# Kernel optimization log

Hardware: AMD Instinct MI355X
Metric: run time of the kernel (lower is better)

The kernel has to match this reference:

```python
import jax, jax.numpy as jnp
import numpy as np

N, M = 50000, 24
F_NODE_IN, F_EDGE_IN = 92, 41
F, E = 64, 64  # node_fea_len, edge_fea_len


def _kaiming(key, fan_in, fan_out):
    # kaiming_uniform_(mode='fan_in', nonlinearity='relu'): bound = sqrt(6/fan_in)
    bound = np.sqrt(6.0 / fan_in)
    return jax.random.uniform(key, (fan_in, fan_out), jnp.float32, -bound, bound)


def setup_inputs() -> dict:
    key = jax.random.key(0)
    ks = jax.random.split(key, 10)
    node_fea = jax.random.normal(ks[0], (N, F_NODE_IN), jnp.float32)
    edge_fea = jax.random.normal(ks[1], (N, M, F_EDGE_IN), jnp.float32)
    # indices in [-1, N-1); -1 marks padded neighbors (masked), matching torch semantics
    edge_fea_idx = jax.random.randint(ks[2], (N, M), 0, N + 1, jnp.int64 if jax.config.jax_enable_x64 else jnp.int32) - 1
    inp = {
        'node_fea': node_fea,
        'edge_fea': edge_fea,
        'edge_fea_idx': edge_fea_idx,
        'Wn': _kaiming(ks[3], F_NODE_IN, F), 'bn': jnp.zeros((F,), jnp.float32),
        'We': _kaiming(ks[4], F_EDGE_IN, E), 'be': jnp.zeros((E,), jnp.float32),
    }
    for i, k in zip((1, 2, 3), ks[5:8]):
        inp[f'W{i}'] = _kaiming(k, 2 * F + E, 2 * F)
        inp[f'b{i}'] = jnp.zeros((2 * F,), jnp.float32)
        inp[f'a{i}'] = jnp.float32(0.7)
    return inp


def conv_layer(node, edge, idx, W, b, alpha):
    n, m = idx.shape
    nbr = node[idx]  # (N, M, F) gather; negative idx wraps like torch, masked below
    self_fea = jnp.broadcast_to(node[:, None, :], (n, m, node.shape[-1]))
    total = jnp.concatenate([self_fea, nbr, edge], axis=2)  # (N, M, 2F+E)
    gated = total @ W + b  # (N, M, 2F)
    nbr_filter, nbr_core = jnp.split(gated, 2, axis=2)
    mask = (idx >= 0)[:, :, None].astype(node.dtype)
    prod = jax.nn.sigmoid(nbr_filter) * jax.nn.softplus(nbr_core) * mask
    nbr_sumed = jnp.sum(prod, axis=1)  # (N, F)
    return jax.nn.softplus(alpha * node + nbr_sumed)


def reference(node_fea, edge_fea, edge_fea_idx, Wn, bn, We, be,
              W1, b1, a1, W2, b2, a2, W3, b3, a3):
    node = node_fea @ Wn + bn            # (N, 64)
    edge = edge_fea @ We + be            # (N, M, 64)
    node = conv_layer(node, edge, edge_fea_idx, W1, b1, a1)
    node = conv_layer(node, edge, edge_fea_idx, W2, b2, a2)
    node = conv_layer(node, edge, edge_fea_idx, W3, b3, a3)
    return node
```

## Files before the change

### kernel.cpp

```cpp
#include <hip/hip_runtime.h>
#include <cstdint>
#include <cstddef>

#define NN   50000
#define MM   24
#define FNIN 92
#define FEIN 41
#define NBLK 3125
#define EROW 48
#define ETILE (MM * 16 * EROW)
#define LOG2E 1.4426950408889634f
#define LN2   0.6931471805599453f

typedef __attribute__((ext_vector_type(8))) short bf16x8;
typedef __attribute__((ext_vector_type(4))) float f32x4;
typedef __attribute__((ext_vector_type(8))) unsigned short u16x8;
typedef __attribute__((ext_vector_type(2))) _Float16 f16x2;

__device__ __forceinline__ unsigned short f2bf(float x) {
    unsigned int u = __float_as_uint(x);
    return (unsigned short)((u + 0x7fffu + ((u >> 16) & 1u)) >> 16);
}
__device__ __forceinline__ float bf2f(unsigned short h) {
    return __uint_as_float(((unsigned int)h) << 16);
}
__device__ __forceinline__ _Float16 f2h_clamp(float x) {
    return (_Float16)fminf(fmaxf(x, -60000.f), 60000.f);
}
__device__ __forceinline__ float exp2f_fast(float x) {
#if __has_builtin(__builtin_amdgcn_exp2f)
    return __builtin_amdgcn_exp2f(x);
#else
    float r; asm("v_exp_f32 %0, %1" : "=v"(r) : "v"(x)); return r;
#endif
}
__device__ __forceinline__ float log2f_fast(float x) {
#if __has_builtin(__builtin_amdgcn_logf)
    return __builtin_amdgcn_logf(x);
#else
    float r; asm("v_log_f32 %0, %1" : "=v"(r) : "v"(x)); return r;
#endif
}


__global__ __launch_bounds__(256) void prep_kernel(
    const float* __restrict__ We, const float* __restrict__ be,
    const float* __restrict__ W1, const float* __restrict__ b1,
    const float* __restrict__ W2, const float* __restrict__ b2,
    const float* __restrict__ W3, const float* __restrict__ b3,
    unsigned short* __restrict__ WcB,
    unsigned short* __restrict__ WsnBhi, unsigned short* __restrict__ WsnBlo,
    float* __restrict__ bias_c, _Float16* __restrict__ Pn)
{
    __shared__ float Wu_s[64 * 128];
    __shared__ float We_s[FEIN * 64];
    int l = blockIdx.x / 24;
    int part = blockIdx.x % 24;
    const float* W  = (l == 0) ? W1 : (l == 1) ? W2 : W3;
    const float* bl = (l == 0) ? b1 : (l == 1) ? b2 : b3;
    int tid = threadIdx.x;
    if (blockIdx.x == 0 && tid < 128) {
        Pn[(size_t)NN * 128 + tid] = (tid & 1) ? (_Float16)0.f : (_Float16)(-60000.f);
    }
    if (part < 8) {
        for (int i = tid; i < 64 * 128; i += 256) Wu_s[i] = W[128 * 128 + i];
        for (int i = tid; i < FEIN * 64; i += 256) We_s[i] = We[i];
        __syncthreads();
        int j = part;
        for (int e = tid; e < 1024; e += 256) {
            int s = e >> 9, L = (e >> 3) & 63, t = e & 7;
            int k = s * 32 + ((L >> 4) << 3) + t;
            int n = 16 * j + (L & 15);
            float v = 0.f;
            if (k < FEIN) {
                for (int i = 0; i < 64; ++i)
                    v += We_s[k * 64 + i] * Wu_s[i * 128 + n];
            }
            WcB[l * 8192 + j * 1024 + e] = f2bf(v * LOG2E);
        }
        if (part == 0 && tid < 128) {
            float v = bl[tid];
            for (int i = 0; i < 64; ++i)
                v += be[i] * Wu_s[i * 128 + tid];
            bias_c[l * 128 + tid] = v * LOG2E;
        }
    } else {
        int j = part - 8;
        for (int e = tid; e < 1024; e += 256) {
            int s = e >> 9, L = (e >> 3) & 63, t = e & 7;
            int k = s * 32 + ((L >> 4) << 3) + t;
            int n = 16 * j + (L & 15);
            float v = (n < 128) ? W[k * 128 + n] : W[(64 + k) * 128 + (n - 128)];
            v *= LOG2E;
            unsigned short h = f2bf(v);
            WsnBhi[l * 16384 + j * 1024 + e] = h;
            WsnBlo[l * 16384 + j * 1024 + e] = f2bf(v - bf2f(h));
        }
    }
}

#define CN 8
__global__ __launch_bounds__(256) void cast_kernel(
    const float* __restrict__ edge_fea, unsigned short* __restrict__ edge_tiles)
{
    __shared__ float s[CN * MM * FEIN];
    int B = blockIdx.x;
    int b = B >> 1, half = B & 1;
    const float4* src = (const float4*)(edge_fea + ((size_t)b * 16 + half * CN) * (MM * FEIN));
    float4* sd = (float4*)s;
    for (int i = threadIdx.x; i < (CN * MM * FEIN) / 4; i += 256)
        sd[i] = src[i];
    __syncthreads();
    unsigned short* dst = edge_tiles + (size_t)b * ETILE;
    for (int c = threadIdx.x; c < CN * MM * 6; c += 256) {
        int r = c / 6, cc = c - r * 6;
        int m = r >> 3, nbl = r & 7;
        int k0 = cc * 8;
        const float* srow = &s[(nbl * MM + m) * FEIN];
        u16x8 v;
        #pragma unroll
        for (int j = 0; j < 8; ++j) {
            int k = k0 + j;
            v[j] = (k < FEIN) ? f2bf(srow[k]) : (unsigned short)0;
        }
        *(u16x8*)(dst + (size_t)(m * 16 + half * CN + nbl) * EROW + k0) = v;
    }
}

__global__ __launch_bounds__(256) void embed_kernel(
    const float* __restrict__ node_fea, const float* __restrict__ Wn,
    const float* __restrict__ bn, float* __restrict__ node_out)
{
    __shared__ float w_s[FNIN * 64];
    __shared__ float f_s[64 * FNIN];
    int tid = threadIdx.x;
    int base = blockIdx.x * 64;
    int cnt = min(64, NN - base);
    for (int i = tid; i < FNIN * 64; i += 256) w_s[i] = Wn[i];
    for (int i = tid; i < cnt * FNIN; i += 256) f_s[i] = node_fea[base * FNIN + i];
    __syncthreads();
    int c = tid & 63, g = tid >> 6;
    float acc[16];
    #pragma unroll
    for (int jj = 0; jj < 16; ++jj) acc[jj] = 0.f;
    for (int k = 0; k < FNIN; ++k) {
        float wv = w_s[k * 64 + c];
        #pragma unroll
        for (int jj = 0; jj < 16; ++jj)
            acc[jj] += f_s[(g + 4 * jj) * FNIN + k] * wv;
    }
    float bv = bn[c];
    #pragma unroll
    for (int jj = 0; jj < 16; ++jj) {
        int n = g + 4 * jj;
        if (n < cnt) node_out[(base + n) * 64 + c] = acc[jj] + bv;
    }
}

__global__ __launch_bounds__(256) void p_kernel(
    const float* __restrict__ node,
    const unsigned short* __restrict__ Bhi, const unsigned short* __restrict__ Blo,
    _Float16* __restrict__ Ps, _Float16* __restrict__ Pn)
{
    __shared__ float n_s[64 * 68];
    int tid = threadIdx.x;
    int base = blockIdx.x * 64;
    int cnt = min(64, NN - base);
    for (int i = tid; i < cnt * 64; i += 256) {
        int r = i >> 6, c = i & 63;
        n_s[r * 68 + c] = node[base * 64 + i];
    }
    __syncthreads();
    int w = tid >> 6, L = tid & 63, quad = L >> 4, lc = L & 15;
    const float* ap = &n_s[(16 * w + lc) * 68 + quad * 8];
    bf16x8 a0h, a0l, a1h, a1l;
    for (int t = 0; t < 8; ++t) {
        float x0 = ap[t];
        float x1 = ap[32 + t];
        unsigned short h0 = f2bf(x0), h1 = f2bf(x1);
        a0h[t] = (short)h0; a1h[t] = (short)h1;
        a0l[t] = (short)f2bf(x0 - bf2f(h0));
        a1l[t] = (short)f2bf(x1 - bf2f(h1));
    }
    const bf16x8* bh = (const bf16x8*)Bhi;
    const bf16x8* bl = (const bf16x8*)Blo;
    #pragma unroll
    for (int jp = 0; jp < 8; ++jp) {
        int jf = (jp < 4) ? jp : (jp + 4);
        int jc = jf + 4;
        bf16x8 f0h = bh[(jf * 2 + 0) * 64 + L];
        bf16x8 f1h = bh[(jf * 2 + 1) * 64 + L];
        bf16x8 f0l = bl[(jf * 2 + 0) * 64 + L];
        bf16x8 f1l = bl[(jf * 2 + 1) * 64 + L];
        bf16x8 c0h = bh[(jc * 2 + 0) * 64 + L];
        bf16x8 c1h = bh[(jc * 2 + 1) * 64 + L];
        bf16x8 c0l = bl[(jc * 2 + 0) * 64 + L];
        bf16x8 c1l = bl[(jc * 2 + 1) * 64 + L];
        f32x4 Cf = {0.f, 0.f, 0.f, 0.f}, Cc = {0.f, 0.f, 0.f, 0.f};
        Cf = __builtin_amdgcn_mfma_f32_16x16x32_bf16(a0h, f0h, Cf, 0, 0, 0);
        Cf = __builtin_amdgcn_mfma_f32_16x16x32_bf16(a1h, f1h, Cf, 0, 0, 0);
        Cf = __builtin_amdgcn_mfma_f32_16x16x32_bf16(a0l, f0h, Cf, 0, 0, 0);
        Cf = __builtin_amdgcn_mfma_f32_16x16x32_bf16(a1l, f1h, Cf, 0, 0, 0);
        Cf = __builtin_amdgcn_mfma_f32_16x16x32_bf16(a0h, f0l, Cf, 0, 0, 0);
        Cf = __builtin_amdgcn_mfma_f32_16x16x32_bf16(a1h, f1l, Cf, 0, 0, 0);
        Cc = __builtin_amdgcn_mfma_f32_16x16x32_bf16(a0h, c0h, Cc, 0, 0, 0);
        Cc = __builtin_amdgcn_mfma_f32_16x16x32_bf16(a1h, c1h, Cc, 0, 0, 0);
        Cc = __builtin_amdgcn_mfma_f32_16x16x32_bf16(a0l, c0h, Cc, 0, 0, 0);
        Cc = __builtin_amdgcn_mfma_f32_16x16x32_bf16(a1l, c1h, Cc, 0, 0, 0);
        Cc = __builtin_amdgcn_mfma_f32_16x16x32_bf16(a0h, c0l, Cc, 0, 0, 0);
        Cc = __builtin_amdgcn_mfma_f32_16x16x32_bf16(a1h, c1l, Cc, 0, 0, 0);
        int cl = (jp < 4) ? (16 * jp + lc) : (16 * (jp - 4) + lc);
        _Float16* P = (jp < 4) ? Ps : Pn;
        #pragma unroll
        for (int r = 0; r < 4; ++r) {
            int nr = 16 * w + quad * 4 + r;
            if (nr < cnt) {
                f16x2 v = {f2h_clamp(Cf[r]), f2h_clamp(Cc[r])};
                *(f16x2*)&P[(size_t)(base + nr) * 128 + 2 * cl] = v;
            }
        }
    }
}

__global__ __launch_bounds__(256, 5) void conv_kernel(
    const float* __restrict__ node_in, const int* __restrict__ idx,
    const unsigned short* __restrict__ edge_tiles,
    const _Float16* __restrict__ Ps, const _Float16* __restrict__ Pn,
    const unsigned short* __restrict__ WcB, const float* __restrict__ bias_c,
    const float* __restrict__ alpha_p, float* __restrict__ node_out)
{
    __shared__ unsigned ofs_s[16 * 25];
    int tid = threadIdx.x;
    int b = blockIdx.x;
    int base = b * 16;
    for (int i = tid; i < 16 * MM; i += 256) {
        int row = i / MM, m = i - row * MM;
        int g = idx[base * MM + i];
        unsigned gg = (unsigned)((g >= 0) ? g : NN);
        ofs_s[row * 25 + m] = gg << 8;
    }
    if (tid < 16) ofs_s[tid * 25 + 24] = ((unsigned)NN) << 8;
    __syncthreads();

    int w = tid >> 6, L = tid & 63, quad = L >> 4, lc = L & 15;
    int colf = 16 * w + lc;
    const bf16x8* wcb = (const bf16x8*)WcB;
    bf16x8 bf0 = wcb[(w * 2 + 0) * 64 + L];
    bf16x8 bf1 = wcb[(w * 2 + 1) * 64 + L];
    bf16x8 bc0 = wcb[((w + 4) * 2 + 0) * 64 + L];
    bf16x8 bc1 = wcb[((w + 4) * 2 + 1) * 64 + L];

    float bias_f = bias_c[colf];
    float bias_g = bias_c[64 + colf];
    float psb_f[4], psb_c[4];
    #pragma unroll
    for (int r = 0; r < 4; ++r) {
        int nr = base + quad * 4 + r;
        f16x2 sp = *(const f16x2*)&Ps[(size_t)nr * 128 + 2 * colf];
        psb_f[r] = (float)sp[0] + bias_f;
        psb_c[r] = (float)sp[1] + bias_g;
    }

    float acc[4] = {0.f, 0.f, 0.f, 0.f};
    const char* PnB = (const char*)Pn;
    unsigned coff = (unsigned)colf << 2;
    const unsigned* ofsr = &ofs_s[quad * 100];
    const unsigned short* et = edge_tiles + (size_t)b * ETILE + lc * EROW + quad * 8;

    auto conv_step = [&](const f16x2 (&PN)[4], bf16x8 A0, bf16x8 A1) {
        f32x4 Cf = {psb_f[0], psb_f[1], psb_f[2], psb_f[3]};
        f32x4 Cc = {psb_c[0], psb_c[1], psb_c[2], psb_c[3]};
        Cf = __builtin_amdgcn_mfma_f32_16x16x32_bf16(A0, bf0, Cf, 0, 0, 0);
        Cf = __builtin_amdgcn_mfma_f32_16x16x32_bf16(A1, bf1, Cf, 0, 0, 0);
        Cc = __builtin_amdgcn_mfma_f32_16x16x32_bf16(A0, bc0, Cc, 0, 0, 0);
        Cc = __builtin_amdgcn_mfma_f32_16x16x32_bf16(A1, bc1, Cc, 0, 0, 0);
        #pragma unroll
        for (int r = 0; r < 4; ++r) {
            float gf = Cf[r] + (float)PN[r][0];
            float gc = Cc[r] + (float)PN[r][1];
            float sg = __builtin_amdgcn_rcpf(1.0f + exp2f_fast(-gf));
            float sp2 = fmaxf(gc, 0.f)
                      + log2f_fast(1.0f + exp2f_fast(fminf(gc, -gc)));
            acc[r] = fmaf(sg, sp2, acc[r]);
        }
    };

    unsigned o1[4], o2[4], o3[4];
    f16x2 pnA[4], pnB[4];
    {
        unsigned o0[4];
        #pragma unroll
        for (int r = 0; r < 4; ++r) o0[r] = ofsr[r * 25 + 0];
        #pragma unroll
        for (int r = 0; r < 4; ++r)
            pnA[r] = *(const f16x2*)(PnB + (o0[r] + coff));
    }
    bf16x8 aA0 = *(const bf16x8*)(et);
    bf16x8 aA1 = *(const bf16x8*)(et + 32);
    #pragma unroll
    for (int r = 0; r < 4; ++r) o1[r] = ofsr[r * 25 + 1];
    #pragma unroll
    for (int r = 0; r < 4; ++r) o2[r] = ofsr[r * 25 + 2];
    bf16x8 aB0, aB1;

    #pragma unroll 1
    for (int t = 0; t < 12; ++t) {
        int m = 2 * t;
        #pragma unroll
        for (int r = 0; r < 4; ++r)
            pnB[r] = *(const f16x2*)(PnB + (o1[r] + coff));
        {
            const unsigned short* ep = et + (m + 1) * 768;
            aB0 = *(const bf16x8*)(ep);
            aB1 = *(const bf16x8*)(ep + 32);
        }
        int m3 = min(m + 3, 24);
        #pragma unroll
        for (int r = 0; r < 4; ++r) o3[r] = ofsr[r * 25 + m3];
        conv_step(pnA, aA0, aA1);
        #pragma unroll
        for (int r = 0; r < 4; ++r)
            pnA[r] = *(const f16x2*)(PnB + (o2[r] + coff));
        {
            int me = min(m + 2, 23);
            const unsigned short* ep = et + me * 768;
            aA0 = *(const bf16x8*)(ep);
            aA1 = *(const bf16x8*)(ep + 32);
        }
        int m4 = min(m + 4, 24);
        #pragma unroll
        for (int r = 0; r < 4; ++r) o2[r] = ofsr[r * 25 + m4];
        conv_step(pnB, aB0, aB1);
        #pragma unroll
        for (int r = 0; r < 4; ++r) o1[r] = o3[r];
    }

    float alpha = alpha_p[0];
    #pragma unroll
    for (int r = 0; r < 4; ++r) {
        int nr = base + quad * 4 + r;
        float x = alpha * node_in[nr * 64 + colf] + acc[r] * LN2;
        float o = fmaxf(x, 0.f) + __logf(1.0f + __expf(-fabsf(x)));
        node_out[nr * 64 + colf] = o;
    }
}

extern "C" void kernel_launch(void* const* d_in, const int* in_sizes, int n_in,
                              void* d_out, int out_size, void* d_ws, size_t ws_size,
                              hipStream_t stream)
{
    const float* node_fea = (const float*)d_in[0];
    const float* edge_fea = (const float*)d_in[1];
    const int*   eidx     = (const int*)d_in[2];
    const float* Wn = (const float*)d_in[3];
    const float* bn = (const float*)d_in[4];
    const float* We = (const float*)d_in[5];
    const float* be = (const float*)d_in[6];
    const float* W1 = (const float*)d_in[7];
    const float* b1 = (const float*)d_in[8];
    const float* a1 = (const float*)d_in[9];
    const float* W2 = (const float*)d_in[10];
    const float* b2 = (const float*)d_in[11];
    const float* a2 = (const float*)d_in[12];
    const float* W3 = (const float*)d_in[13];
    const float* b3 = (const float*)d_in[14];
    const float* a3 = (const float*)d_in[15];
    float* out = (float*)d_out;

    char* ws = (char*)d_ws;
    unsigned short* edge_tiles = (unsigned short*)ws;
    size_t off = 115200256;
    float* nodeA = (float*)(ws + off); off += 12800000;
    float* nodeB = (float*)(ws + off); off += 12800000;
    _Float16* Ps = (_Float16*)(ws + off); off += 12800000;
    _Float16* Pn = (_Float16*)(ws + off); off += 12800256;
    unsigned short* WcB    = (unsigned short*)(ws + off); off += 3 * 8192 * 2;
    unsigned short* WsnBhi = (unsigned short*)(ws + off); off += 3 * 16384 * 2;
    unsigned short* WsnBlo = (unsigned short*)(ws + off); off += 3 * 16384 * 2;
    float* bias_c = (float*)(ws + off); off += 3 * 128 * 4;

    prep_kernel<<<dim3(72), dim3(256), 0, stream>>>(We, be, W1, b1, W2, b2, W3, b3,
                                                    WcB, WsnBhi, WsnBlo, bias_c, Pn);
    cast_kernel<<<dim3(2 * NBLK), dim3(256), 0, stream>>>(edge_fea, edge_tiles);
    embed_kernel<<<dim3(782), dim3(256), 0, stream>>>(node_fea, Wn, bn, nodeA);

    p_kernel<<<dim3(782), dim3(256), 0, stream>>>(nodeA, WsnBhi, WsnBlo, Ps, Pn);
    conv_kernel<<<dim3(NBLK), dim3(256), 0, stream>>>(nodeA, eidx, edge_tiles, Ps, Pn,
                                                      WcB, bias_c, a1, nodeB);

    p_kernel<<<dim3(782), dim3(256), 0, stream>>>(nodeB, WsnBhi + 16384, WsnBlo + 16384, Ps, Pn);
    conv_kernel<<<dim3(NBLK), dim3(256), 0, stream>>>(nodeB, eidx, edge_tiles, Ps, Pn,
                                                      WcB + 8192, bias_c + 128, a2, nodeA);

    p_kernel<<<dim3(782), dim3(256), 0, stream>>>(nodeA, WsnBhi + 32768, WsnBlo + 32768, Ps, Pn);
    conv_kernel<<<dim3(NBLK), dim3(256), 0, stream>>>(nodeA, eidx, edge_tiles, Ps, Pn,
                                                      WcB + 16384, bias_c + 256, a3, out);
}
```

Before: 622.2 us.

## Deepen conv gather prefetch to four neighbor stages and relax occupancy

Restructures the conv kernel's neighbor loop from a two-stage to a four-stage software pipeline. Gathered Pn values, edge tiles and LDS offsets are kept in flight for four neighbors ahead, which is meant to hide the latency of the random gathers. To make room for the extra registers, launch bounds drop from 5 to 4 blocks per CU. The LDS offset table is padded to a stride of 32 so that look-ahead slots past the last neighbor point at the padded dummy row. The workspace offset is bumped so that edge-tile over-reads on the last block stay in bounds. The trade-off is more register pressure and lower occupancy in exchange for more memory-level parallelism per wave.

```diff
diff --git a/kernel.cpp b/kernel.cpp
--- a/kernel.cpp
+++ b/kernel.cpp
@@ -222,24 +222,26 @@
     }
 }
 
-__global__ __launch_bounds__(256, 5) void conv_kernel(
+__global__ __launch_bounds__(256, 4) void conv_kernel(
     const float* __restrict__ node_in, const int* __restrict__ idx,
     const unsigned short* __restrict__ edge_tiles,
     const _Float16* __restrict__ Ps, const _Float16* __restrict__ Pn,
     const unsigned short* __restrict__ WcB, const float* __restrict__ bias_c,
     const float* __restrict__ alpha_p, float* __restrict__ node_out)
 {
-    __shared__ unsigned ofs_s[16 * 25];
+    __shared__ unsigned ofs_s[16 * 32];
     int tid = threadIdx.x;
     int b = blockIdx.x;
     int base = b * 16;
-    for (int i = tid; i < 16 * MM; i += 256) {
-        int row = i / MM, m = i - row * MM;
-        int g = idx[base * MM + i];
-        unsigned gg = (unsigned)((g >= 0) ? g : NN);
-        ofs_s[row * 25 + m] = gg << 8;
-    }
-    if (tid < 16) ofs_s[tid * 25 + 24] = ((unsigned)NN) << 8;
+    for (int i = tid; i < 16 * 32; i += 256) {
+        int row = i >> 5, m = i & 31;
+        unsigned gg = (unsigned)NN;
+        if (m < MM) {
+            int g = idx[base * MM + row * MM + m];
+            gg = (unsigned)((g >= 0) ? g : NN);
+        }
+        ofs_s[i] = gg << 8;
+    }
     __syncthreads();
 
     int w = tid >> 6, L = tid & 63, quad = L >> 4, lc = L & 15;
@@ -264,7 +266,7 @@
     float acc[4] = {0.f, 0.f, 0.f, 0.f};
     const char* PnB = (const char*)Pn;
     unsigned coff = (unsigned)colf << 2;
-    const unsigned* ofsr = &ofs_s[quad * 100];
+    const unsigned* ofsr = &ofs_s[quad * 4 * 32];
     const unsigned short* et = edge_tiles + (size_t)b * ETILE + lc * EROW + quad * 8;
 
     auto conv_step = [&](const f16x2 (&PN)[4], bf16x8 A0, bf16x8 A1) {
@@ -284,55 +286,52 @@
             acc[r] = fmaf(sg, sp2, acc[r]);
         }
     };
-
-    unsigned o1[4], o2[4], o3[4];
-    f16x2 pnA[4], pnB[4];
-    {
-        unsigned o0[4];
-        #pragma unroll
-        for (int r = 0; r < 4; ++r) o0[r] = ofsr[r * 25 + 0];
+    auto val_load = [&](f16x2 (&PN)[4], const unsigned (&O)[4]) {
         #pragma unroll
         for (int r = 0; r < 4; ++r)
-            pnA[r] = *(const f16x2*)(PnB + (o0[r] + coff));
-    }
-    bf16x8 aA0 = *(const bf16x8*)(et);
-    bf16x8 aA1 = *(const bf16x8*)(et + 32);
-    #pragma unroll
-    for (int r = 0; r < 4; ++r) o1[r] = ofsr[r * 25 + 1];
-    #pragma unroll
-    for (int r = 0; r < 4; ++r) o2[r] = ofsr[r * 25 + 2];
-    bf16x8 aB0, aB1;
+            PN[r] = *(const f16x2*)(PnB + (O[r] + coff));
+    };
+    auto edg_load = [&](bf16x8& A0, bf16x8& A1, int m) {
+        const unsigned short* ep = et + m * 768;
+        A0 = *(const bf16x8*)(ep);
+        A1 = *(const bf16x8*)(ep + 32);
+    };
+    auto ofs_read = [&](unsigned (&O)[4], int slot) {
+        #pragma unroll
+        for (int r = 0; r < 4; ++r) O[r] = ofsr[r * 32 + slot];
+    };
+
+    unsigned o0[4], o1[4], o2[4], o3[4];
+    f16x2 pn0[4], pn1[4], pn2[4], pn3[4];
+    bf16x8 a0_0, a0_1, a1_0, a1_1, a2_0, a2_1, a3_0, a3_1;
+
+    ofs_read(o0, 0); ofs_read(o1, 1); ofs_read(o2, 2); ofs_read(o3, 3);
+    val_load(pn0, o0); val_load(pn1, o1); val_load(pn2, o2); val_load(pn3, o3);
+    edg_load(a0_0, a0_1, 0); edg_load(a1_0, a1_1, 1);
+    edg_load(a2_0, a2_1, 2); edg_load(a3_0, a3_1, 3);
+    ofs_read(o0, 4); ofs_read(o1, 5);
 
     #pragma unroll 1
-    for (int t = 0; t < 12; ++t) {
-        int m = 2 * t;
-        #pragma unroll
-        for (int r = 0; r < 4; ++r)
-            pnB[r] = *(const f16x2*)(PnB + (o1[r] + coff));
-        {
-            const unsigned short* ep = et + (m + 1) * 768;
-            aB0 = *(const bf16x8*)(ep);
-            aB1 = *(const bf16x8*)(ep + 32);
-        }
-        int m3 = min(m + 3, 24);
-        #pragma unroll
-        for (int r = 0; r < 4; ++r) o3[r] = ofsr[r * 25 + m3];
-        conv_step(pnA, aA0, aA1);
-        #pragma unroll
-        for (int r = 0; r < 4; ++r)
-            pnA[r] = *(const f16x2*)(PnB + (o2[r] + coff));
-        {
-            int me = min(m + 2, 23);
-            const unsigned short* ep = et + me * 768;
-            aA0 = *(const bf16x8*)(ep);
-            aA1 = *(const bf16x8*)(ep + 32);
-        }
-        int m4 = min(m + 4, 24);
-        #pragma unroll
-        for (int r = 0; r < 4; ++r) o2[r] = ofsr[r * 25 + m4];
-        conv_step(pnB, aB0, aB1);
-        #pragma unroll
-        for (int r = 0; r < 4; ++r) o1[r] = o3[r];
+    for (int tt = 0; tt < 6; ++tt) {
+        int m = 4 * tt;
+        int mE = min(m + 4, 24), mO = min(m + 5, 24);
+        conv_step(pn0, a0_0, a0_1);
+        val_load(pn0, o0);
+        edg_load(a0_0, a0_1, mE);
+        ofs_read(o2, m + 6);
+        conv_step(pn1, a1_0, a1_1);
+        val_load(pn1, o1);
+        edg_load(a1_0, a1_1, mO);
+        ofs_read(o3, m + 7);
+        int mE2 = min(m + 6, 24), mO2 = min(m + 7, 24);
+        conv_step(pn2, a2_0, a2_1);
+        val_load(pn2, o2);
+        edg_load(a2_0, a2_1, mE2);
+        ofs_read(o0, m + 8);
+        conv_step(pn3, a3_0, a3_1);
+        val_load(pn3, o3);
+        edg_load(a3_0, a3_1, mO2);
+        ofs_read(o1, m + 9);
     }
 
     float alpha = alpha_p[0];
@@ -369,7 +368,7 @@
 
     char* ws = (char*)d_ws;
     unsigned short* edge_tiles = (unsigned short*)ws;
-    size_t off = 115200256;
+    size_t off = 115204352;
     float* nodeA = (float*)(ws + off); off += 12800000;
     float* nodeB = (float*)(ws + off); off += 12800000;
     _Float16* Ps = (_Float16*)(ws + off); off += 12800000;
```

New measurement: 640.7 us. 1.03x slower.

## Fuse next-layer projection into conv epilogue and embed kernel

Applied to the files above, without the earlier changes.

Removes the standalone p_kernel launches. The node projection (Ps/Pn) for the next layer is now computed in each conv block's epilogue from its own output rows, and in the embed kernel for the first layer. Ps/Pn are double-buffered so the next layer's tables can be written while the current layer's neighbour gathers still read the old ones. This saves three launches and a re-read of the node array, at the cost of extra workspace and more registers, LDS and MFMA work at the tail of conv_kernel, which may lower its occupancy.

```diff
diff --git a/kernel.cpp b/kernel.cpp
--- a/kernel.cpp
+++ b/kernel.cpp
@@ -50,7 +50,8 @@
     const float* __restrict__ W3, const float* __restrict__ b3,
     unsigned short* __restrict__ WcB,
     unsigned short* __restrict__ WsnBhi, unsigned short* __restrict__ WsnBlo,
-    float* __restrict__ bias_c, _Float16* __restrict__ Pn)
+    float* __restrict__ bias_c, _Float16* __restrict__ PnA,
+    _Float16* __restrict__ PnB)
 {
     __shared__ float Wu_s[64 * 128];
     __shared__ float We_s[FEIN * 64];
@@ -60,7 +61,9 @@
     const float* bl = (l == 0) ? b1 : (l == 1) ? b2 : b3;
     int tid = threadIdx.x;
     if (blockIdx.x == 0 && tid < 128) {
-        Pn[(size_t)NN * 128 + tid] = (tid & 1) ? (_Float16)0.f : (_Float16)(-60000.f);
+        _Float16 sv = (tid & 1) ? (_Float16)0.f : (_Float16)(-60000.f);
+        PnA[(size_t)NN * 128 + tid] = sv;
+        PnB[(size_t)NN * 128 + tid] = sv;
     }
     if (part < 8) {
         for (int i = tid; i < 64 * 128; i += 256) Wu_s[i] = W[128 * 128 + i];
@@ -127,9 +130,11 @@
     }
 }
 
-__global__ __launch_bounds__(256) void embed_kernel(
+__global__ __launch_bounds__(256) void embed_p_kernel(
     const float* __restrict__ node_fea, const float* __restrict__ Wn,
-    const float* __restrict__ bn, float* __restrict__ node_out)
+    const float* __restrict__ bn, float* __restrict__ node_out,
+    const unsigned short* __restrict__ Bhi, const unsigned short* __restrict__ Blo,
+    _Float16* __restrict__ Ps, _Float16* __restrict__ Pn)
 {
     __shared__ float w_s[FNIN * 64];
     __shared__ float f_s[64 * FNIN];
@@ -150,29 +155,19 @@
             acc[jj] += f_s[(g + 4 * jj) * FNIN + k] * wv;
     }
     float bv = bn[c];
+    __syncthreads();
+    float* x_s = w_s;
     #pragma unroll
     for (int jj = 0; jj < 16; ++jj) {
         int n = g + 4 * jj;
-        if (n < cnt) node_out[(base + n) * 64 + c] = acc[jj] + bv;
-    }
-}
-
-__global__ __launch_bounds__(256) void p_kernel(
-    const float* __restrict__ node,
-    const unsigned short* __restrict__ Bhi, const unsigned short* __restrict__ Blo,
-    _Float16* __restrict__ Ps, _Float16* __restrict__ Pn)
-{
-    __shared__ float n_s[64 * 68];
-    int tid = threadIdx.x;
-    int base = blockIdx.x * 64;
-    int cnt = min(64, NN - base);
-    for (int i = tid; i < cnt * 64; i += 256) {
-        int r = i >> 6, c = i & 63;
-        n_s[r * 68 + c] = node[base * 64 + i];
+        float v = acc[jj] + bv;
+        if (n < cnt) node_out[(base + n) * 64 + c] = v;
+        x_s[n * 68 + c] = v;
     }
     __syncthreads();
+
     int w = tid >> 6, L = tid & 63, quad = L >> 4, lc = L & 15;
-    const float* ap = &n_s[(16 * w + lc) * 68 + quad * 8];
+    const float* ap = &x_s[(16 * w + lc) * 68 + quad * 8];
     bf16x8 a0h, a0l, a1h, a1l;
     for (int t = 0; t < 8; ++t) {
         float x0 = ap[t];
@@ -227,9 +222,12 @@
     const unsigned short* __restrict__ edge_tiles,
     const _Float16* __restrict__ Ps, const _Float16* __restrict__ Pn,
     const unsigned short* __restrict__ WcB, const float* __restrict__ bias_c,
-    const float* __restrict__ alpha_p, float* __restrict__ node_out)
+    const float* __restrict__ alpha_p, float* __restrict__ node_out,
+    const unsigned short* __restrict__ NBhi, const unsigned short* __restrict__ NBlo,
+    _Float16* __restrict__ Ps_out, _Float16* __restrict__ Pn_out)
 {
     __shared__ unsigned ofs_s[16 * 25];
+    __shared__ float x_s[16 * 68];
     int tid = threadIdx.x;
     int b = blockIdx.x;
     int base = b * 16;
@@ -262,7 +260,7 @@
     }
 
     float acc[4] = {0.f, 0.f, 0.f, 0.f};
-    const char* PnB = (const char*)Pn;
+    const char* PnB_ = (const char*)Pn;
     unsigned coff = (unsigned)colf << 2;
     const unsigned* ofsr = &ofs_s[quad * 100];
     const unsigned short* et = edge_tiles + (size_t)b * ETILE + lc * EROW + quad * 8;
@@ -293,7 +291,7 @@
         for (int r = 0; r < 4; ++r) o0[r] = ofsr[r * 25 + 0];
         #pragma unroll
         for (int r = 0; r < 4; ++r)
-            pnA[r] = *(const f16x2*)(PnB + (o0[r] + coff));
+            pnA[r] = *(const f16x2*)(PnB_ + (o0[r] + coff));
     }
     bf16x8 aA0 = *(const bf16x8*)(et);
     bf16x8 aA1 = *(const bf16x8*)(et + 32);
@@ -308,7 +306,7 @@
         int m = 2 * t;
         #pragma unroll
         for (int r = 0; r < 4; ++r)
-            pnB[r] = *(const f16x2*)(PnB + (o1[r] + coff));
+            pnB[r] = *(const f16x2*)(PnB_ + (o1[r] + coff));
         {
             const unsigned short* ep = et + (m + 1) * 768;
             aB0 = *(const bf16x8*)(ep);
@@ -320,7 +318,7 @@
         conv_step(pnA, aA0, aA1);
         #pragma unroll
         for (int r = 0; r < 4; ++r)
-            pnA[r] = *(const f16x2*)(PnB + (o2[r] + coff));
+            pnA[r] = *(const f16x2*)(PnB_ + (o2[r] + coff));
         {
             int me = min(m + 2, 23);
             const unsigned short* ep = et + me * 768;
@@ -342,6 +340,58 @@
         float x = alpha * node_in[nr * 64 + colf] + acc[r] * LN2;
         float o = fmaxf(x, 0.f) + __logf(1.0f + __expf(-fabsf(x)));
         node_out[nr * 64 + colf] = o;
+        x_s[(quad * 4 + r) * 68 + colf] = o;
+    }
+
+    if (Ps_out) {
+        __syncthreads();
+        const float* ap = &x_s[lc * 68 + quad * 8];
+        bf16x8 a0h, a0l, a1h, a1l;
+        for (int t = 0; t < 8; ++t) {
+            float x0 = ap[t];
+            float x1 = ap[32 + t];
+            unsigned short h0 = f2bf(x0), h1 = f2bf(x1);
+            a0h[t] = (short)h0; a1h[t] = (short)h1;
+            a0l[t] = (short)f2bf(x0 - bf2f(h0));
+            a1l[t] = (short)f2bf(x1 - bf2f(h1));
+        }
+        const bf16x8* bh = (const bf16x8*)NBhi;
+        const bf16x8* bl = (const bf16x8*)NBlo;
+        #pragma unroll
+        for (int u = 0; u < 2; ++u) {
+            int jp = 2 * w + u;
+            int jf = (jp < 4) ? jp : (jp + 4);
+            int jc = jf + 4;
+            bf16x8 f0h = bh[(jf * 2 + 0) * 64 + L];
+            bf16x8 f1h = bh[(jf * 2 + 1) * 64 + L];
+            bf16x8 f0l = bl[(jf * 2 + 0) * 64 + L];
+            bf16x8 f1l = bl[(jf * 2 + 1) * 64 + L];
+            bf16x8 c0h = bh[(jc * 2 + 0) * 64 + L];
+            bf16x8 c1h = bh[(jc * 2 + 1) * 64 + L];
+            bf16x8 c0l = bl[(jc * 2 + 0) * 64 + L];
+            bf16x8 c1l = bl[(jc * 2 + 1) * 64 + L];
+            f32x4 Cf = {0.f, 0.f, 0.f, 0.f}, Cc = {0.f, 0.f, 0.f, 0.f};
+            Cf = __builtin_amdgcn_mfma_f32_16x16x32_bf16(a0h, f0h, Cf, 0, 0, 0);
+            Cf = __builtin_amdgcn_mfma_f32_16x16x32_bf16(a1h, f1h, Cf, 0, 0, 0);
+            Cf = __builtin_amdgcn_mfma_f32_16x16x32_bf16(a0l, f0h, Cf, 0, 0, 0);
+            Cf = __builtin_amdgcn_mfma_f32_16x16x32_bf16(a1l, f1h, Cf, 0, 0, 0);
+            Cf = __builtin_amdgcn_mfma_f32_16x16x32_bf16(a0h, f0l, Cf, 0, 0, 0);
+            Cf = __builtin_amdgcn_mfma_f32_16x16x32_bf16(a1h, f1l, Cf, 0, 0, 0);
+            Cc = __builtin_amdgcn_mfma_f32_16x16x32_bf16(a0h, c0h, Cc, 0, 0, 0);
+            Cc = __builtin_amdgcn_mfma_f32_16x16x32_bf16(a1h, c1h, Cc, 0, 0, 0);
+            Cc = __builtin_amdgcn_mfma_f32_16x16x32_bf16(a0l, c0h, Cc, 0, 0, 0);
+            Cc = __builtin_amdgcn_mfma_f32_16x16x32_bf16(a1l, c1h, Cc, 0, 0, 0);
+            Cc = __builtin_amdgcn_mfma_f32_16x16x32_bf16(a0h, c0l, Cc, 0, 0, 0);
+            Cc = __builtin_amdgcn_mfma_f32_16x16x32_bf16(a1h, c1l, Cc, 0, 0, 0);
+            int cl = (jp < 4) ? (16 * jp + lc) : (16 * (jp - 4) + lc);
+            _Float16* P = (jp < 4) ? Ps_out : Pn_out;
+            #pragma unroll
+            for (int r = 0; r < 4; ++r) {
+                int nr = quad * 4 + r;
+                f16x2 v = {f2h_clamp(Cf[r]), f2h_clamp(Cc[r])};
+                *(f16x2*)&P[(size_t)(base + nr) * 128 + 2 * cl] = v;
+            }
+        }
     }
 }
 
@@ -369,30 +419,34 @@
 
     char* ws = (char*)d_ws;
     unsigned short* edge_tiles = (unsigned short*)ws;
-    size_t off = 115200256;
+    size_t off = 115204352;
     float* nodeA = (float*)(ws + off); off += 12800000;
     float* nodeB = (float*)(ws + off); off += 12800000;
-    _Float16* Ps = (_Float16*)(ws + off); off += 12800000;
-    _Float16* Pn = (_Float16*)(ws + off); off += 12800256;
+    _Float16* PsA = (_Float16*)(ws + off); off += 12800000;
+    _Float16* PnA = (_Float16*)(ws + off); off += 12800256;
+    _Float16* PsB = (_Float16*)(ws + off); off += 12800000;
+    _Float16* PnB = (_Float16*)(ws + off); off += 12800256;
     unsigned short* WcB    = (unsigned short*)(ws + off); off += 3 * 8192 * 2;
     unsigned short* WsnBhi = (unsigned short*)(ws + off); off += 3 * 16384 * 2;
     unsigned short* WsnBlo = (unsigned short*)(ws + off); off += 3 * 16384 * 2;
     float* bias_c = (float*)(ws + off); off += 3 * 128 * 4;
 
     prep_kernel<<<dim3(72), dim3(256), 0, stream>>>(We, be, W1, b1, W2, b2, W3, b3,
-                                                    WcB, WsnBhi, WsnBlo, bias_c, Pn);
+                                                    WcB, WsnBhi, WsnBlo, bias_c,
+                                                    PnA, PnB);
     cast_kernel<<<dim3(2 * NBLK), dim3(256), 0, stream>>>(edge_fea, edge_tiles);
-    embed_kernel<<<dim3(782), dim3(256), 0, stream>>>(node_fea, Wn, bn, nodeA);
-
-    p_kernel<<<dim3(782), dim3(256), 0, stream>>>(nodeA, WsnBhi, WsnBlo, Ps, Pn);
-    conv_kernel<<<dim3(NBLK), dim3(256), 0, stream>>>(nodeA, eidx, edge_tiles, Ps, Pn,
-                                                      WcB, bias_c, a1, nodeB);
-
-    p_kernel<<<dim3(782), dim3(256), 0, stream>>>(nodeB, WsnBhi + 16384, WsnBlo + 16384, Ps, Pn);
-    conv_kernel<<<dim3(NBLK), dim3(256), 0, stream>>>(nodeB, eidx, edge_tiles, Ps, Pn,
-                                                      WcB + 8192, bias_c + 128, a2, nodeA);
-
-    p_kernel<<<dim3(782), dim3(256), 0, stream>>>(nodeA, WsnBhi + 32768, WsnBlo + 32768, Ps, Pn);
-    conv_kernel<<<dim3(NBLK), dim3(256), 0, stream>>>(nodeA, eidx, edge_tiles, Ps, Pn,
-                                                      WcB + 16384, bias_c + 256, a3, out);
-}
+
+    embed_p_kernel<<<dim3(782), dim3(256), 0, stream>>>(node_fea, Wn, bn, nodeA,
+                                                        WsnBhi, WsnBlo, PsA, PnA);
+    conv_kernel<<<dim3(NBLK), dim3(256), 0, stream>>>(nodeA, eidx, edge_tiles, PsA, PnA,
+                                                      WcB, bias_c, a1, nodeB,
+                                                      WsnBhi + 16384, WsnBlo + 16384,
+                                                      PsB, PnB);
+    conv_kernel<<<dim3(NBLK), dim3(256), 0, stream>>>(nodeB, eidx, edge_tiles, PsB, PnB,
+                                                      WcB + 8192, bias_c + 128, a2, nodeA,
+                                                      WsnBhi + 32768, WsnBlo + 32768,
+                                                      PsA, PnA);
+    conv_kernel<<<dim3(NBLK), dim3(256), 0, stream>>>(nodeA, eidx, edge_tiles, PsA, PnA,
+                                                      WcB + 16384, bias_c + 256, a3, out,
+                                                      nullptr, nullptr, nullptr, nullptr);
+}
```

Measured after the change: 601.4 us. 3.3% less time.
